# Kernel optimization log

Hardware: AMD Instinct MI355X
Metric: run time of the kernel (lower is better)

## Reference

```python
import jax, jax.numpy as jnp
import numpy as np
from jax import lax

N_EMBD = 1024
N_HEAD = 16
HEAD_DIM = N_EMBD // N_HEAD
EPS = 1e-6
B, T = 4, 2048


def setup_inputs() -> dict:
    key = jax.random.key(0)
    ks = jax.random.split(key, 5)
    scale = 1.0 / np.sqrt(N_EMBD)
    return {
        "x": jax.random.normal(ks[0], (B, T, N_EMBD), jnp.float32),
        "W_attn": jax.random.normal(ks[1], (N_EMBD, 3 * N_EMBD), jnp.float32) * scale,
        "b_attn": jax.random.normal(ks[2], (3 * N_EMBD,), jnp.float32) * 0.01,
        "W_proj": jax.random.normal(ks[3], (N_EMBD, N_EMBD), jnp.float32) * scale,
        "b_proj": jax.random.normal(ks[4], (N_EMBD,), jnp.float32) * 0.01,
    }


def _feature_map(x):
    # ELU + 1 for non-negativity
    return jax.nn.elu(x) + 1.0


def reference(x, W_attn, b_attn, W_proj, b_proj):
    Bb, Tt, C = x.shape
    qkv = x @ W_attn + b_attn  # (B,T,3C)
    q, k, v = jnp.split(qkv, 3, axis=-1)

    def to_heads(t):
        # (B,T,C) -> (T,B,H,d): scan axis leading
        return t.reshape(Bb, Tt, N_HEAD, HEAD_DIM).transpose(1, 0, 2, 3)

    q = _feature_map(to_heads(q))
    k = _feature_map(to_heads(k))
    v = to_heads(v)

    # Causal linear attention: O(d^2) running state instead of the torch
    # code's materialized (B,H,T,d,d) cumsum — same math.
    def step(carry, inp):
        kv, ksum = carry  # (B,H,d,d), (B,H,d)
        qt, kt, vt = inp  # each (B,H,d)
        kv = kv + kt[..., :, None] * vt[..., None, :]
        ksum = ksum + kt
        num = jnp.einsum('bhi,bhij->bhj', qt, kv)
        den = jnp.einsum('bhi,bhi->bh', qt, ksum)[..., None] + EPS
        return (kv, ksum), num / den

    init = (
        jnp.zeros((Bb, N_HEAD, HEAD_DIM, HEAD_DIM), x.dtype),
        jnp.zeros((Bb, N_HEAD, HEAD_DIM), x.dtype),
    )
    _, y = lax.scan(step, init, (q, k, v))  # (T,B,H,d)
    y = y.transpose(1, 0, 2, 3).reshape(Bb, Tt, C)
    return y @ W_proj + b_proj  # dropout is identity in eval mode
```

## Files before the change

kernel.cpp:

```cpp
#include <hip/hip_runtime.h>
#include <math.h>

#define BB   4
#define TT   2048
#define CC   1024
#define HH   16
#define DD   64
#define MM   (BB*TT)
#define NQKV (3*CC)
#define LCH  128
#define NCH  (TT/LCH)
#define EPSF 1e-6f

#define QKST 72
#define PST  136
#define VTST 136

typedef __bf16 bf16x8 __attribute__((ext_vector_type(8)));
typedef float  floatx4 __attribute__((ext_vector_type(4)));

__device__ __forceinline__ unsigned short f2bf(float f) {
  union { float f; unsigned int u; } v; v.f = f;
  unsigned int r = v.u + 0x7fffu + ((v.u >> 16) & 1u);
  return (unsigned short)(r >> 16);
}
__device__ __forceinline__ float bf2f(unsigned short s) {
  union { unsigned int u; float f; } v; v.u = ((unsigned int)s) << 16;
  return v.f;
}
__device__ __forceinline__ float featmap(float v) {
  return v > 0.f ? v + 1.f : __expf(v);
}
__device__ __forceinline__ void gld_lds_b128(const unsigned short* g, unsigned short* l) {
  __builtin_amdgcn_global_load_lds(
      (const __attribute__((address_space(1))) unsigned int*)g,
      (__attribute__((address_space(3))) unsigned int*)l, 16, 0, 0);
}

__device__ __forceinline__ void transpose_cvt_body(const float* __restrict__ W,
                                                   unsigned short* __restrict__ out,
                                                   int R, int Cc, int bx32, int by32, int tid) {
  __shared__ float tile[32][33];
  int tx = tid & 31, ty = tid >> 5;
  int bx = bx32 * 32, by = by32 * 32;
  #pragma unroll
  for (int i = ty; i < 32; i += 8)
    tile[i][tx] = W[(size_t)(by + i) * Cc + bx + tx];
  __syncthreads();
  #pragma unroll
  for (int i = ty; i < 32; i += 8)
    out[(size_t)(bx + i) * R + by + tx] = f2bf(tile[tx][i]);
}

__global__ __launch_bounds__(256) void prep_kernel(
    const float* __restrict__ x, unsigned short* __restrict__ xb,
    const float* __restrict__ Wa, unsigned short* __restrict__ WaT,
    const float* __restrict__ Wp, unsigned short* __restrict__ WpT) {
  int blk = blockIdx.x, tid = threadIdx.x;
  if (blk < 8192) {
    int i = (blk * 256 + tid) * 4;
    float4 f = *(const float4*)(x + i);
    ushort4 o;
    o.x = f2bf(f.x); o.y = f2bf(f.y); o.z = f2bf(f.z); o.w = f2bf(f.w);
    *(ushort4*)(xb + i) = o;
  } else if (blk < 8192 + 3072) {
    int t = blk - 8192;
    transpose_cvt_body(Wa, WaT, CC, NQKV, t % 96, t / 96, tid);
  } else {
    int t = blk - 11264;
    transpose_cvt_body(Wp, WpT, CC, CC, t % 32, t / 32, tid);
  }
}

#define GEMM_K_LOOP(A_, Bt_, K_)                                                 \
  __shared__ __align__(16) unsigned short As[128 * 64];                          \
  __shared__ __align__(16) unsigned short Bs[128 * 64];                          \
  int tid = threadIdx.x;                                                         \
  int wave = tid >> 6, lane = tid & 63;                                          \
  int lr = lane & 15, lq = lane >> 4;                                            \
  int m0 = blockIdx.y * 128, n0 = blockIdx.x * 128;                              \
  int wm = (wave >> 1) * 64, wn = (wave & 1) * 64;                               \
  int lrow = lane >> 3;                        \
  int lk = (lane & 7) ^ lrow;                       \
  int rbase = wave * 32;                                                         \
  const unsigned short* gA = A_ + (size_t)(m0 + rbase + lrow) * K_ + lk * 8;     \
  const unsigned short* gB = Bt_ + (size_t)(n0 + rbase + lrow) * K_ + lk * 8;    \
  unsigned short* lA = As + rbase * 64;                                          \
  unsigned short* lB = Bs + rbase * 64;                                          \
  floatx4 acc[4][4] = {};                                                        \
  for (int k0 = 0; k0 < K_; k0 += 64) {                                          \
    __syncthreads();                 \
    _Pragma("unroll")                                                            \
    for (int g = 0; g < 4; g++) {                                                \
      gld_lds_b128(gA + k0 + (size_t)g * 8 * K_, lA + g * 512);                  \
      gld_lds_b128(gB + k0 + (size_t)g * 8 * K_, lB + g * 512);                  \
    }                                                                            \
    __syncthreads();                                    \
    _Pragma("unroll")                                                            \
    for (int kk = 0; kk < 2; kk++) {                                             \
      bf16x8 an[4], bm[4];                                                       \
      _Pragma("unroll")                                                          \
      for (int i = 0; i < 4; i++)                                                \
        an[i] = *(const bf16x8*)&Bs[(wn + i * 16 + lr) * 64 + ((((kk << 2) + lq) ^ (lr & 7)) << 3)]; \
      _Pragma("unroll")                                                          \
      for (int j = 0; j < 4; j++)                                                \
        bm[j] = *(const bf16x8*)&As[(wm + j * 16 + lr) * 64 + ((((kk << 2) + lq) ^ (lr & 7)) << 3)]; \
      _Pragma("unroll")                                                          \
      for (int i = 0; i < 4; i++)                                                \
        _Pragma("unroll")                                                        \
        for (int j = 0; j < 4; j++)                                              \
          acc[i][j] = __builtin_amdgcn_mfma_f32_16x16x32_bf16(an[i], bm[j], acc[i][j], 0, 0, 0); \
    }                                                                            \
  }

#define BKQ   32
#define QSLOT (256 * BKQ)
#define NT_Q  (CC / BKQ)

__global__ __launch_bounds__(512, 2) void gemm_qkv_kernel(
    const unsigned short* __restrict__ A, const unsigned short* __restrict__ Bt,
    const float* __restrict__ bias,
    unsigned short* __restrict__ qh, unsigned short* __restrict__ kh,
    unsigned short* __restrict__ vh) {
  extern __shared__ __align__(16) unsigned short lds[];
  unsigned short* Asr = lds;
  unsigned short* Bsr = lds + 4 * QSLOT;

  const int tid = threadIdx.x;
  const int wave = tid >> 6, lane = tid & 63;
  const int lr = lane & 15, lq = lane >> 4;
  const int m0 = blockIdx.y * 256, n0 = blockIdx.x * 256;
  const int wm = (wave >> 2) * 128, wn = (wave & 3) * 64;

  const int srow = wave * 16 + (lane >> 2);
  const int cs = (lane & 3) ^ ((lane >> 3) & 3);
  const unsigned short* gA = A  + (size_t)(m0 + srow) * CC + cs * 8;
  const unsigned short* gB = Bt + (size_t)(n0 + srow) * CC + cs * 8;
  unsigned short* const stA = Asr + wave * 512;
  unsigned short* const stB = Bsr + wave * 512;

  const int chunk = lq ^ ((lr >> 1) & 3);
  const int roA = (wm + lr) * BKQ + chunk * 8;
  const int roB = (wn + lr) * BKQ + chunk * 8;

  floatx4 acc[4][8] = {};

#define QSTAGE_A(tt) do {                                      \
    const unsigned short* g_ = gA + (tt) * BKQ;                \
    unsigned short* d_ = stA + ((tt) & 3) * QSLOT;             \
    gld_lds_b128(g_, d_);                                      \
    gld_lds_b128(g_ + (size_t)128 * CC, d_ + 128 * BKQ);       \
  } while (0)
#define QSTAGE_B(tt) do {                                      \
    const unsigned short* g_ = gB + (tt) * BKQ;                \
    unsigned short* d_ = stB + ((tt) & 3) * QSLOT;             \
    gld_lds_b128(g_, d_);                                      \
    gld_lds_b128(g_ + (size_t)128 * CC, d_ + 128 * BKQ);       \
  } while (0)

  QSTAGE_A(0); QSTAGE_B(0);
  QSTAGE_A(1); QSTAGE_B(1);
  QSTAGE_A(2); QSTAGE_B(2);
  asm volatile("s_waitcnt vmcnt(8)" ::: "memory");
  __builtin_amdgcn_s_barrier();

  #pragma unroll 4
  for (int t = 0; t < NT_Q; ++t) {
    const unsigned short* sA = Asr + (t & 3) * QSLOT + roA;
    const unsigned short* sB = Bsr + (t & 3) * QSLOT + roB;
    bf16x8 an[4], bm[4], bm2[4];
    #pragma unroll
    for (int i = 0; i < 4; i++) an[i] = *(const bf16x8*)(sB + i * (16 * BKQ));
    #pragma unroll
    for (int j = 0; j < 4; j++) bm[j] = *(const bf16x8*)(sA + j * (16 * BKQ));
    if (t < NT_Q - 3) QSTAGE_A(t + 3);
    __builtin_amdgcn_s_barrier();
    __builtin_amdgcn_s_setprio(1);
    #pragma unroll
    for (int i = 0; i < 4; i++)
      #pragma unroll
      for (int j = 0; j < 4; j++)
        acc[i][j] = __builtin_amdgcn_mfma_f32_16x16x32_bf16(an[i], bm[j], acc[i][j], 0, 0, 0);
    __builtin_amdgcn_s_setprio(0);
    #pragma unroll
    for (int j = 0; j < 4; j++) bm2[j] = *(const bf16x8*)(sA + (4 + j) * (16 * BKQ));
    if (t < NT_Q - 3) QSTAGE_B(t + 3);
    if (t < NT_Q - 3) {
      asm volatile("s_waitcnt vmcnt(8) lgkmcnt(0)" ::: "memory");
      __builtin_amdgcn_s_barrier();
    } else if (t == NT_Q - 3) {
      asm volatile("s_waitcnt vmcnt(4) lgkmcnt(0)" ::: "memory");
      __builtin_amdgcn_s_barrier();
    } else if (t == NT_Q - 2) {
      asm volatile("s_waitcnt vmcnt(0) lgkmcnt(0)" ::: "memory");
      __builtin_amdgcn_s_barrier();
    }
    __builtin_amdgcn_s_setprio(1);
    #pragma unroll
    for (int i = 0; i < 4; i++)
      #pragma unroll
      for (int j = 0; j < 4; j++)
        acc[i][4 + j] = __builtin_amdgcn_mfma_f32_16x16x32_bf16(an[i], bm2[j], acc[i][4 + j], 0, 0, 0);
    __builtin_amdgcn_s_setprio(0);
  }
#undef QSTAGE_A
#undef QSTAGE_B

  const int which = n0 >> 10;
  unsigned short* dst = (which == 0) ? qh : (which == 1) ? kh : vh;
  #pragma unroll
  for (int i = 0; i < 4; i++) {
    const int n = n0 + wn + i * 16 + lq * 4;
    const int h = (n & 1023) >> 6, dd = n & 63;
    const float4 bi = *(const float4*)&bias[n];
    #pragma unroll
    for (int j = 0; j < 8; j++) {
      const int m = m0 + wm + j * 16 + lr;
      const int b = m >> 11, tg = m & 2047;
      float v0 = acc[i][j][0] + bi.x, v1 = acc[i][j][1] + bi.y;
      float v2 = acc[i][j][2] + bi.z, v3 = acc[i][j][3] + bi.w;
      if (which < 2) { v0 = featmap(v0); v1 = featmap(v1); v2 = featmap(v2); v3 = featmap(v3); }
      ushort4 o; o.x = f2bf(v0); o.y = f2bf(v1); o.z = f2bf(v2); o.w = f2bf(v3);
      *(ushort4*)&dst[(((size_t)(b * HH + h)) * TT + tg) * DD + dd] = o;
    }
  }
}

__global__ __launch_bounds__(256) void gemm_proj_kernel(
    const unsigned short* __restrict__ A, const unsigned short* __restrict__ Bt,
    const float* __restrict__ bias, float* __restrict__ out) {
  GEMM_K_LOOP(A, Bt, CC)
  #pragma unroll
  for (int i = 0; i < 4; i++) {
    int n = n0 + wn + i * 16 + lq * 4;
    float4 bi = *(const float4*)&bias[n];
    #pragma unroll
    for (int j = 0; j < 4; j++) {
      int m = m0 + wm + j * 16 + lr;
      float4 o;
      o.x = acc[i][j][0] + bi.x; o.y = acc[i][j][1] + bi.y;
      o.z = acc[i][j][2] + bi.z; o.w = acc[i][j][3] + bi.w;
      *(float4*)&out[(size_t)m * CC + n] = o;
    }
  }
}

__global__ __launch_bounds__(256) void chunk_state_kernel(
    const unsigned short* __restrict__ kh, const unsigned short* __restrict__ vh,
    float* __restrict__ KVx) {
  __shared__ __align__(16) unsigned short Kt[64 * VTST];
  __shared__ __align__(16) unsigned short Vt[80 * VTST];
  int blk = blockIdx.x;
  int bh = blk / NCH, c = blk % NCH;
  int tid = threadIdx.x;
  const unsigned short* kp = kh + ((size_t)bh * TT + c * LCH) * DD;
  const unsigned short* vp = vh + ((size_t)bh * TT + c * LCH) * DD;
  {
    int t = tid & 127;
    for (int j8 = (tid >> 7) * 8; j8 < DD; j8 += 16) {
      union { uint4 u; unsigned short s[8]; } wk, wv;
      wk.u = *(const uint4*)&kp[(size_t)t * DD + j8];
      wv.u = *(const uint4*)&vp[(size_t)t * DD + j8];
      #pragma unroll
      for (int jj = 0; jj < 8; jj++) {
        Kt[(j8 + jj) * VTST + t] = wk.s[jj];
        Vt[(j8 + jj) * VTST + t] = wv.s[jj];
      }
    }
  }
  for (int e = tid; e < 16 * 128; e += 256) {
    int rr = e >> 7, n = e & 127;
    Vt[(64 + rr) * VTST + n] = (rr == 0) ? (unsigned short)0x3F80 : (unsigned short)0;
  }
  __syncthreads();
  int wave = tid >> 6, lane = tid & 63;
  int lr = lane & 15, lq = lane >> 4;
  int i0 = wave * 16;
  floatx4 acc[5] = {};
  #pragma unroll
  for (int kk = 0; kk < 4; kk++) {
    bf16x8 a = *(const bf16x8*)&Kt[(i0 + lr) * VTST + kk * 32 + lq * 8];
    #pragma unroll
    for (int jt = 0; jt < 5; jt++) {
      bf16x8 b = *(const bf16x8*)&Vt[(jt * 16 + lr) * VTST + kk * 32 + lq * 8];
      acc[jt] = __builtin_amdgcn_mfma_f32_16x16x32_bf16(a, b, acc[jt], 0, 0, 0);
    }
  }
  float* o = KVx + (size_t)blk * 5120;
  #pragma unroll
  for (int jt = 0; jt < 5; jt++)
    *(float4*)&o[(jt * 16 + lr) * 64 + i0 + lq * 4] = *(float4*)&acc[jt];
}

__global__ __launch_bounds__(256) void prefix_state_kernel(const float* __restrict__ KVx,
                                                           unsigned short* __restrict__ SPb) {
  int bh = blockIdx.x / 5, jb = blockIdx.x % 5;
  int e = jb * 1024 + threadIdx.x * 4;
  float run0 = 0.f, run1 = 0.f, run2 = 0.f, run3 = 0.f;
  for (int c = 0; c < NCH; c++) {
    size_t base = ((size_t)bh * NCH + c) * 5120 + e;
    float4 v = *(const float4*)&KVx[base];
    ushort4 o;
    o.x = f2bf(run0); o.y = f2bf(run1); o.z = f2bf(run2); o.w = f2bf(run3);
    *(ushort4*)&SPb[base] = o;
    run0 += v.x; run1 += v.y; run2 += v.z; run3 += v.w;
  }
}

__global__ __launch_bounds__(256) void chunk_attn_kernel(
    const unsigned short* __restrict__ qh, const unsigned short* __restrict__ kh,
    const unsigned short* __restrict__ vh, const unsigned short* __restrict__ SPb,
    unsigned short* __restrict__ yb) {
  __shared__ __align__(16) unsigned short lds[128 * QKST * 2 + 80 * VTST];
  unsigned short* Qs = lds;
  unsigned short* Ks = lds + 128 * QKST;
  unsigned short* P  = lds;
  unsigned short* Vt = lds + 128 * QKST * 2;

  int blk = blockIdx.x;
  int bh = blk / NCH, c = blk % NCH;
  int b = bh / HH, h = bh % HH;
  int tid = threadIdx.x;
  const unsigned short* qp = qh + ((size_t)bh * TT + c * LCH) * DD;
  const unsigned short* kp = kh + ((size_t)bh * TT + c * LCH) * DD;
  const unsigned short* vp = vh + ((size_t)bh * TT + c * LCH) * DD;

  for (int e = tid; e < 1024; e += 256) {
    int row = e >> 3, k8 = (e & 7) * 8;
    *(uint4*)&Qs[row * QKST + k8] = *(const uint4*)&qp[(size_t)row * DD + k8];
    *(uint4*)&Ks[row * QKST + k8] = *(const uint4*)&kp[(size_t)row * DD + k8];
  }
  {
    int t = tid & 127;
    for (int j8 = (tid >> 7) * 8; j8 < DD; j8 += 16) {
      union { uint4 u; unsigned short s[8]; } w;
      w.u = *(const uint4*)&vp[(size_t)t * DD + j8];
      #pragma unroll
      for (int jj = 0; jj < 8; jj++) Vt[(j8 + jj) * VTST + t] = w.s[jj];
    }
  }
  for (int e = tid; e < 16 * 128; e += 256) {
    int rr = e >> 7, n = e & 127;
    Vt[(64 + rr) * VTST + n] = (rr == 0) ? (unsigned short)0x3F80 : (unsigned short)0;
  }
  __syncthreads();

  int wave = tid >> 6, lane = tid & 63;
  int lr = lane & 15, lq = lane >> 4;
  int mbase = wave * 32;

  bf16x8 aq[2][2];
  #pragma unroll
  for (int i = 0; i < 2; i++)
    #pragma unroll
    for (int kk = 0; kk < 2; kk++)
      aq[i][kk] = *(const bf16x8*)&Qs[(mbase + i * 16 + lr) * QKST + kk * 32 + lq * 8];

  floatx4 accT[5][2] = {};
  const unsigned short* spb = SPb + (size_t)blk * (80 * 64);
  #pragma unroll
  for (int jt = 0; jt < 5; jt++)
    #pragma unroll
    for (int kk = 0; kk < 2; kk++) {
      bf16x8 asp = *(const bf16x8*)&spb[(jt * 16 + lr) * 64 + kk * 32 + lq * 8];
      accT[jt][0] = __builtin_amdgcn_mfma_f32_16x16x32_bf16(asp, aq[0][kk], accT[jt][0], 0, 0, 0);
      accT[jt][1] = __builtin_amdgcn_mfma_f32_16x16x32_bf16(asp, aq[1][kk], accT[jt][1], 0, 0, 0);
    }
  floatx4 sacc[2][8] = {};
  #pragma unroll
  for (int nt = 0; nt < 8; nt++)
    #pragma unroll
    for (int kk = 0; kk < 2; kk++) {
      bf16x8 bk = *(const bf16x8*)&Ks[(nt * 16 + lr) * QKST + kk * 32 + lq * 8];
      sacc[0][nt] = __builtin_amdgcn_mfma_f32_16x16x32_bf16(aq[0][kk], bk, sacc[0][nt], 0, 0, 0);
      sacc[1][nt] = __builtin_amdgcn_mfma_f32_16x16x32_bf16(aq[1][kk], bk, sacc[1][nt], 0, 0, 0);
    }
  __syncthreads();

  #pragma unroll
  for (int i = 0; i < 2; i++)
    #pragma unroll
    for (int nt = 0; nt < 8; nt++) {
      int col = nt * 16 + lr;
      #pragma unroll
      for (int r = 0; r < 4; r++) {
        int m = mbase + i * 16 + lq * 4 + r;
        float v = (col <= m) ? sacc[i][nt][r] : 0.f;
        P[m * PST + col] = f2bf(v);
      }
    }
  __syncthreads();

  #pragma unroll
  for (int kk4 = 0; kk4 < 4; kk4++) {
    bf16x8 bp0 = *(const bf16x8*)&P[(mbase + lr) * PST + kk4 * 32 + lq * 8];
    bf16x8 bp1 = *(const bf16x8*)&P[(mbase + 16 + lr) * PST + kk4 * 32 + lq * 8];
    #pragma unroll
    for (int jt = 0; jt < 5; jt++) {
      bf16x8 av = *(const bf16x8*)&Vt[(jt * 16 + lr) * VTST + kk4 * 32 + lq * 8];
      accT[jt][0] = __builtin_amdgcn_mfma_f32_16x16x32_bf16(av, bp0, accT[jt][0], 0, 0, 0);
      accT[jt][1] = __builtin_amdgcn_mfma_f32_16x16x32_bf16(av, bp1, accT[jt][1], 0, 0, 0);
    }
  }

  #pragma unroll
  for (int it = 0; it < 2; it++) {
    float den = __shfl(accT[4][it][0], lr, 64);
    float inv = 1.f / (den + EPSF);
    int tg = c * LCH + mbase + it * 16 + lr;
    size_t base = ((size_t)b * TT + tg) * CC + h * DD;
    #pragma unroll
    for (int jt = 0; jt < 4; jt++) {
      ushort4 o;
      o.x = f2bf(accT[jt][it][0] * inv);
      o.y = f2bf(accT[jt][it][1] * inv);
      o.z = f2bf(accT[jt][it][2] * inv);
      o.w = f2bf(accT[jt][it][3] * inv);
      *(ushort4*)&yb[base + jt * 16 + lq * 4] = o;
    }
  }
}

extern "C" void kernel_launch(void* const* d_in, const int* in_sizes, int n_in,
                              void* d_out, int out_size, void* d_ws, size_t ws_size,
                              hipStream_t stream) {
  const float* x      = (const float*)d_in[0];
  const float* W_attn = (const float*)d_in[1];
  const float* b_attn = (const float*)d_in[2];
  const float* W_proj = (const float*)d_in[3];
  const float* b_proj = (const float*)d_in[4];
  float* out = (float*)d_out;

  char* ws = (char*)d_ws;
  size_t off = 0;
  auto alloc = [&](size_t bytes) -> char* {
    char* p = ws + off;
    off += (bytes + 255) & ~(size_t)255;
    return p;
  };
  unsigned short* xb  = (unsigned short*)alloc((size_t)MM * CC * 2);
  unsigned short* WaT = (unsigned short*)alloc((size_t)NQKV * CC * 2);
  unsigned short* WpT = (unsigned short*)alloc((size_t)CC * CC * 2);
  unsigned short* qh  = (unsigned short*)alloc((size_t)MM * CC * 2);
  unsigned short* kh  = (unsigned short*)alloc((size_t)MM * CC * 2);
  unsigned short* vh  = (unsigned short*)alloc((size_t)MM * CC * 2);
  float* KVx = (float*)alloc((size_t)BB * HH * NCH * 80 * 64 * 4);
  unsigned short* SPb = (unsigned short*)alloc((size_t)BB * HH * NCH * 80 * 64 * 2);
  unsigned short* yb = xb;

  static bool s_attr_done = false;
  if (!s_attr_done) {
    (void)hipFuncSetAttribute((const void*)gemm_qkv_kernel,
                              hipFuncAttributeMaxDynamicSharedMemorySize, 131072);
    s_attr_done = true;
  }

  prep_kernel<<<12288, 256, 0, stream>>>(x, xb, W_attn, WaT, W_proj, WpT);
  gemm_qkv_kernel<<<dim3(NQKV / 256, MM / 256), 512, 131072, stream>>>(xb, WaT, b_attn, qh, kh, vh);
  chunk_state_kernel<<<BB * HH * NCH, 256, 0, stream>>>(kh, vh, KVx);
  prefix_state_kernel<<<BB * HH * 5, 256, 0, stream>>>(KVx, SPb);
  chunk_attn_kernel<<<BB * HH * NCH, 256, 0, stream>>>(qh, kh, vh, SPb, yb);
  gemm_proj_kernel<<<dim3(CC / 128, MM / 128), 256, 0, stream>>>(yb, WpT, b_proj, out);
}
```

Before: 236.8 us.

## Retile QKV GEMM to 256x192 blocks and add MFMA priority hints

The QKV GEMM tile changes from 256x256 to 256x192. This gives 16x32=512 blocks instead of 12x32=384, which should balance better across the CUs. Each wave now holds 3x8 accumulators, B staging is partial (only waves 0-3 load the upper half), and the barrier and waitcnt pattern inside the loop is restructured. The epilogue now chooses the destination (q/k/v) per sub-tile, because a 192-wide tile can straddle those boundaries. The chunk_attn MFMA loops are also wrapped in setprio, and the extra barriers add synchronisation cost.

```diff
diff --git a/kernel.cpp b/kernel.cpp
--- a/kernel.cpp
+++ b/kernel.cpp
@@ -114,7 +114,8 @@
   }
 
 #define BKQ   32
-#define QSLOT (256 * BKQ)
+#define ASLT  (256 * BKQ)
+#define BSLT  (192 * BKQ)
 #define NT_Q  (CC / BKQ)
 
 __global__ __launch_bounds__(512, 2) void gemm_qkv_kernel(
@@ -123,105 +124,113 @@
     unsigned short* __restrict__ qh, unsigned short* __restrict__ kh,
     unsigned short* __restrict__ vh) {
   extern __shared__ __align__(16) unsigned short lds[];
-  unsigned short* Asr = lds;
-  unsigned short* Bsr = lds + 4 * QSLOT;
+  unsigned short* Ar = lds;
+  unsigned short* Br = lds + 4 * ASLT;
 
   const int tid = threadIdx.x;
   const int wave = tid >> 6, lane = tid & 63;
   const int lr = lane & 15, lq = lane >> 4;
-  const int m0 = blockIdx.y * 256, n0 = blockIdx.x * 256;
-  const int wm = (wave >> 2) * 128, wn = (wave & 3) * 64;
+  const int m0 = blockIdx.y * 256, n0 = blockIdx.x * 192;
+  const int wm = (wave >> 2) * 128, wn = (wave & 3) * 48;
 
   const int srow = wave * 16 + (lane >> 2);
   const int cs = (lane & 3) ^ ((lane >> 3) & 3);
-  const unsigned short* gA = A  + (size_t)(m0 + srow) * CC + cs * 8;
-  const unsigned short* gB = Bt + (size_t)(n0 + srow) * CC + cs * 8;
-  unsigned short* const stA = Asr + wave * 512;
-  unsigned short* const stB = Bsr + wave * 512;
+  const unsigned short* gA0 = A  + (size_t)(m0 + srow) * CC + cs * 8;
+  const unsigned short* gB0 = Bt + (size_t)(n0 + srow) * CC + cs * 8;
+  unsigned short* const stA = Ar + wave * 512;
+  unsigned short* const stB = Br + wave * 512;
+  const bool bhi = (wave < 4);
 
   const int chunk = lq ^ ((lr >> 1) & 3);
   const int roA = (wm + lr) * BKQ + chunk * 8;
   const int roB = (wn + lr) * BKQ + chunk * 8;
 
-  floatx4 acc[4][8] = {};
+  floatx4 acc[3][8] = {};
 
 #define QSTAGE_A(tt) do {                                      \
-    const unsigned short* g_ = gA + (tt) * BKQ;                \
-    unsigned short* d_ = stA + ((tt) & 3) * QSLOT;             \
+    const unsigned short* g_ = gA0 + (tt) * BKQ;               \
+    unsigned short* d_ = stA + ((tt) & 3) * ASLT;              \
     gld_lds_b128(g_, d_);                                      \
-    gld_lds_b128(g_ + (size_t)128 * CC, d_ + 128 * BKQ);       \
+    gld_lds_b128(g_ + (size_t)128 * CC, d_ + 4096);            \
   } while (0)
 #define QSTAGE_B(tt) do {                                      \
-    const unsigned short* g_ = gB + (tt) * BKQ;                \
-    unsigned short* d_ = stB + ((tt) & 3) * QSLOT;             \
+    const unsigned short* g_ = gB0 + (tt) * BKQ;               \
+    unsigned short* d_ = stB + ((tt) & 3) * BSLT;              \
     gld_lds_b128(g_, d_);                                      \
-    gld_lds_b128(g_ + (size_t)128 * CC, d_ + 128 * BKQ);       \
+    if (bhi) gld_lds_b128(g_ + (size_t)128 * CC, d_ + 4096);   \
   } while (0)
 
   QSTAGE_A(0); QSTAGE_B(0);
   QSTAGE_A(1); QSTAGE_B(1);
   QSTAGE_A(2); QSTAGE_B(2);
-  asm volatile("s_waitcnt vmcnt(8)" ::: "memory");
+  asm volatile("s_waitcnt vmcnt(6)" ::: "memory");
   __builtin_amdgcn_s_barrier();
 
   #pragma unroll 4
   for (int t = 0; t < NT_Q; ++t) {
-    const unsigned short* sA = Asr + (t & 3) * QSLOT + roA;
-    const unsigned short* sB = Bsr + (t & 3) * QSLOT + roB;
-    bf16x8 an[4], bm[4], bm2[4];
-    #pragma unroll
-    for (int i = 0; i < 4; i++) an[i] = *(const bf16x8*)(sB + i * (16 * BKQ));
+    const unsigned short* sA = Ar + (t & 3) * ASLT + roA;
+    const unsigned short* sB = Br + (t & 3) * BSLT + roB;
+    bf16x8 an[3], bm[4], bm2[4];
+    #pragma unroll
+    for (int i = 0; i < 3; i++) an[i] = *(const bf16x8*)(sB + i * (16 * BKQ));
     #pragma unroll
     for (int j = 0; j < 4; j++) bm[j] = *(const bf16x8*)(sA + j * (16 * BKQ));
     if (t < NT_Q - 3) QSTAGE_A(t + 3);
     __builtin_amdgcn_s_barrier();
+    asm volatile("s_waitcnt lgkmcnt(0)" ::: "memory");
     __builtin_amdgcn_s_setprio(1);
     #pragma unroll
-    for (int i = 0; i < 4; i++)
+    for (int i = 0; i < 3; i++)
       #pragma unroll
       for (int j = 0; j < 4; j++)
         acc[i][j] = __builtin_amdgcn_mfma_f32_16x16x32_bf16(an[i], bm[j], acc[i][j], 0, 0, 0);
     __builtin_amdgcn_s_setprio(0);
+    __builtin_amdgcn_s_barrier();
     #pragma unroll
     for (int j = 0; j < 4; j++) bm2[j] = *(const bf16x8*)(sA + (4 + j) * (16 * BKQ));
     if (t < NT_Q - 3) QSTAGE_B(t + 3);
-    if (t < NT_Q - 3) {
-      asm volatile("s_waitcnt vmcnt(8) lgkmcnt(0)" ::: "memory");
-      __builtin_amdgcn_s_barrier();
-    } else if (t == NT_Q - 3) {
-      asm volatile("s_waitcnt vmcnt(4) lgkmcnt(0)" ::: "memory");
-      __builtin_amdgcn_s_barrier();
-    } else if (t == NT_Q - 2) {
-      asm volatile("s_waitcnt vmcnt(0) lgkmcnt(0)" ::: "memory");
-      __builtin_amdgcn_s_barrier();
-    }
+    __builtin_amdgcn_s_barrier();
+    asm volatile("s_waitcnt lgkmcnt(0)" ::: "memory");
     __builtin_amdgcn_s_setprio(1);
     #pragma unroll
-    for (int i = 0; i < 4; i++)
+    for (int i = 0; i < 3; i++)
       #pragma unroll
       for (int j = 0; j < 4; j++)
         acc[i][4 + j] = __builtin_amdgcn_mfma_f32_16x16x32_bf16(an[i], bm2[j], acc[i][4 + j], 0, 0, 0);
     __builtin_amdgcn_s_setprio(0);
+    if (t < NT_Q - 3)        asm volatile("s_waitcnt vmcnt(6)" ::: "memory");
+    else if (t == NT_Q - 3)  asm volatile("s_waitcnt vmcnt(3)" ::: "memory");
+    else if (t == NT_Q - 2)  asm volatile("s_waitcnt vmcnt(0)" ::: "memory");
+    __builtin_amdgcn_s_barrier();
   }
 #undef QSTAGE_A
 #undef QSTAGE_B
 
-  const int which = n0 >> 10;
-  unsigned short* dst = (which == 0) ? qh : (which == 1) ? kh : vh;
-  #pragma unroll
-  for (int i = 0; i < 4; i++) {
+  unsigned short* dstv[3];
+  size_t qoff[3];
+  float4 bi[3];
+  bool feat[3];
+  #pragma unroll
+  for (int i = 0; i < 3; i++) {
     const int n = n0 + wn + i * 16 + lq * 4;
+    dstv[i] = (n < 1024) ? qh : (n < 2048) ? kh : vh;
+    feat[i] = (n < 2048);
     const int h = (n & 1023) >> 6, dd = n & 63;
-    const float4 bi = *(const float4*)&bias[n];
-    #pragma unroll
-    for (int j = 0; j < 8; j++) {
-      const int m = m0 + wm + j * 16 + lr;
-      const int b = m >> 11, tg = m & 2047;
-      float v0 = acc[i][j][0] + bi.x, v1 = acc[i][j][1] + bi.y;
-      float v2 = acc[i][j][2] + bi.z, v3 = acc[i][j][3] + bi.w;
-      if (which < 2) { v0 = featmap(v0); v1 = featmap(v1); v2 = featmap(v2); v3 = featmap(v3); }
+    qoff[i] = (size_t)h * (TT * DD) + dd;
+    bi[i] = *(const float4*)&bias[n];
+  }
+  #pragma unroll
+  for (int j = 0; j < 8; j++) {
+    const int m = m0 + wm + j * 16 + lr;
+    const int b = m >> 11, tg = m & 2047;
+    const size_t pj = (size_t)b * (HH * TT * DD) + (size_t)tg * DD;
+    #pragma unroll
+    for (int i = 0; i < 3; i++) {
+      float v0 = acc[i][j][0] + bi[i].x, v1 = acc[i][j][1] + bi[i].y;
+      float v2 = acc[i][j][2] + bi[i].z, v3 = acc[i][j][3] + bi[i].w;
+      if (feat[i]) { v0 = featmap(v0); v1 = featmap(v1); v2 = featmap(v2); v3 = featmap(v3); }
       ushort4 o; o.x = f2bf(v0); o.y = f2bf(v1); o.z = f2bf(v2); o.w = f2bf(v3);
-      *(ushort4*)&dst[(((size_t)(b * HH + h)) * TT + tg) * DD + dd] = o;
+      *(ushort4*)&dstv[i][pj + qoff[i]] = o;
     }
   }
 }
@@ -358,6 +367,7 @@
 
   floatx4 accT[5][2] = {};
   const unsigned short* spb = SPb + (size_t)blk * (80 * 64);
+  __builtin_amdgcn_s_setprio(1);
   #pragma unroll
   for (int jt = 0; jt < 5; jt++)
     #pragma unroll
@@ -366,7 +376,9 @@
       accT[jt][0] = __builtin_amdgcn_mfma_f32_16x16x32_bf16(asp, aq[0][kk], accT[jt][0], 0, 0, 0);
       accT[jt][1] = __builtin_amdgcn_mfma_f32_16x16x32_bf16(asp, aq[1][kk], accT[jt][1], 0, 0, 0);
     }
+  __builtin_amdgcn_s_setprio(0);
   floatx4 sacc[2][8] = {};
+  __builtin_amdgcn_s_setprio(1);
   #pragma unroll
   for (int nt = 0; nt < 8; nt++)
     #pragma unroll
@@ -375,6 +387,7 @@
       sacc[0][nt] = __builtin_amdgcn_mfma_f32_16x16x32_bf16(aq[0][kk], bk, sacc[0][nt], 0, 0, 0);
       sacc[1][nt] = __builtin_amdgcn_mfma_f32_16x16x32_bf16(aq[1][kk], bk, sacc[1][nt], 0, 0, 0);
     }
+  __builtin_amdgcn_s_setprio(0);
   __syncthreads();
 
   #pragma unroll
@@ -395,12 +408,14 @@
   for (int kk4 = 0; kk4 < 4; kk4++) {
     bf16x8 bp0 = *(const bf16x8*)&P[(mbase + lr) * PST + kk4 * 32 + lq * 8];
     bf16x8 bp1 = *(const bf16x8*)&P[(mbase + 16 + lr) * PST + kk4 * 32 + lq * 8];
+    __builtin_amdgcn_s_setprio(1);
     #pragma unroll
     for (int jt = 0; jt < 5; jt++) {
       bf16x8 av = *(const bf16x8*)&Vt[(jt * 16 + lr) * VTST + kk4 * 32 + lq * 8];
       accT[jt][0] = __builtin_amdgcn_mfma_f32_16x16x32_bf16(av, bp0, accT[jt][0], 0, 0, 0);
       accT[jt][1] = __builtin_amdgcn_mfma_f32_16x16x32_bf16(av, bp1, accT[jt][1], 0, 0, 0);
     }
+    __builtin_amdgcn_s_setprio(0);
   }
 
   #pragma unroll
@@ -451,12 +466,12 @@
   static bool s_attr_done = false;
   if (!s_attr_done) {
     (void)hipFuncSetAttribute((const void*)gemm_qkv_kernel,
-                              hipFuncAttributeMaxDynamicSharedMemorySize, 131072);
+                              hipFuncAttributeMaxDynamicSharedMemorySize, 114688);
     s_attr_done = true;
   }
 
   prep_kernel<<<12288, 256, 0, stream>>>(x, xb, W_attn, WaT, W_proj, WpT);
-  gemm_qkv_kernel<<<dim3(NQKV / 256, MM / 256), 512, 131072, stream>>>(xb, WaT, b_attn, qh, kh, vh);
+  gemm_qkv_kernel<<<dim3(NQKV / 192, MM / 256), 512, 114688, stream>>>(xb, WaT, b_attn, qh, kh, vh);
   chunk_state_kernel<<<BB * HH * NCH, 256, 0, stream>>>(kh, vh, KVx);
   prefix_state_kernel<<<BB * HH * 5, 256, 0, stream>>>(KVx, SPb);
   chunk_attn_kernel<<<BB * HH * NCH, 256, 0, stream>>>(qh, kh, vh, SPb, yb);
```

New measurement: 235.8 us. No clear change (-0.4%).
